# Optimization experiments

Measured on AMD Instinct MI355X. Metric: run time of the kernel, lower is better.

Reference implementation:

```python
import jax, jax.numpy as jnp
import numpy as np

EPS = 1e-8  # torch.cosine_similarity default eps


def setup_inputs() -> dict:
    key = jax.random.key(0)
    k1, k2, k3 = jax.random.split(key, 3)
    B, N, M, C = 8, 2048, 2048, 128
    z = jax.random.randint(k1, (B, N, M), 0, 3, dtype=jnp.int32) - 1  # values in {-1,0,1}
    x1 = jax.random.normal(k2, (B, N, C), dtype=jnp.float32)
    x2 = jax.random.normal(k3, (B, M, C), dtype=jnp.float32)
    s = 10.0
    t = jnp.asarray(s, dtype=jnp.float32)   # nn.Parameter(s)
    b = jnp.asarray(-s, dtype=jnp.float32)  # nn.Parameter(-s)
    return {"z": z, "x1": x1, "x2": x2, "t": t, "b": b}


def reference(z, x1, x2, t, b):
    # cosine similarity as a GEMM instead of broadcast O(B*N*M*C) product:
    # cos = (x1 . x2) / max(||x1|| * ||x2||, eps)  (matches torch.cosine_similarity)
    dots = jnp.einsum('bnc,bmc->bnm', x1, x2)            # [B,N,M]
    n1 = jnp.sqrt(jnp.sum(x1 * x1, axis=-1))             # [B,N]
    n2 = jnp.sqrt(jnp.sum(x2 * x2, axis=-1))             # [B,M]
    denom = jnp.maximum(n1[:, :, None] * n2[:, None, :], EPS)
    cos_sim = dots / denom                               # [B,N,M]

    y = z.astype(jnp.float32) * (t * cos_sim - b)
    mask = z != 0
    nll = -jax.nn.log_sigmoid(y)
    loss = jnp.sum(jnp.where(mask, nll, 0.0)) / jnp.sum(mask).astype(jnp.float32)
    return loss, cos_sim, mask
```

## Files before the change

kernel.cpp:

```cpp
#include <hip/hip_runtime.h>
#include <hip/hip_bf16.h>

#define BATCH 8
#define NDIM  2048
#define MDIM  2048
#define CDIM  128

typedef __attribute__((ext_vector_type(8))) short bf16x8;
typedef __attribute__((ext_vector_type(4))) float f32x4;
typedef __attribute__((ext_vector_type(4), aligned(4))) float f32x4u;

__device__ __forceinline__ float bf2f(unsigned int u16){
    union { unsigned int u; float f; } v; v.u = u16 << 16; return v.f;
}
__device__ __forceinline__ unsigned int f2bf(float f){
    union { float f; unsigned int u; } v; v.f = f;
    unsigned int u = v.u;
    u += 0x7FFFu + ((u >> 16) & 1u);
    return u >> 16;
}

__device__ __forceinline__ void gload_lds16(const void* g, void* l){
    __builtin_amdgcn_global_load_lds(
        (const __attribute__((address_space(1))) void*)g,
        (__attribute__((address_space(3))) void*)l, 16, 0, 0);
}

__global__ void ws_init_kernel(unsigned int* cells){
    cells[threadIdx.x] = 0u;
}

__global__ void finalize_kernel(const float* cells, float* out){
    float s = 0.f;
    int   c = 0;
    #pragma unroll
    for (int i = 0; i < 32; ++i){
        s += cells[i];
        c += ((const int*)cells)[32 + i];
    }
    out[0] = s / (float)c;
}

__global__ __launch_bounds__(256) void prep_kernel(
    const float* __restrict__ x1, const float* __restrict__ x2,
    unsigned short* __restrict__ xb, float* __restrict__ inv)
{
    int gt  = blockIdx.x*256 + threadIdx.x;
    int row = gt >> 4;
    int seg = gt & 15;
    const float* src = (row < 16384) ? (x1 + (size_t)row*128)
                                     : (x2 + (size_t)(row - 16384)*128);
    float4 a = *(const float4*)(src + seg*8);
    float4 b = *(const float4*)(src + seg*8 + 4);
    uint4 pk;
    pk.x = f2bf(a.x) | (f2bf(a.y) << 16);
    pk.y = f2bf(a.z) | (f2bf(a.w) << 16);
    pk.z = f2bf(b.x) | (f2bf(b.y) << 16);
    pk.w = f2bf(b.z) | (f2bf(b.w) << 16);
    ((uint4*)xb)[(size_t)row*16 + seg] = pk;

    float f0 = bf2f(pk.x & 0xffffu), f1 = bf2f(pk.x >> 16);
    float f2 = bf2f(pk.y & 0xffffu), f3 = bf2f(pk.y >> 16);
    float f4 = bf2f(pk.z & 0xffffu), f5 = bf2f(pk.z >> 16);
    float f6 = bf2f(pk.w & 0xffffu), f7 = bf2f(pk.w >> 16);
    float s = f0*f0 + f1*f1 + f2*f2 + f3*f3 + f4*f4 + f5*f5 + f6*f6 + f7*f7;
    s += __shfl_xor(s, 1);
    s += __shfl_xor(s, 2);
    s += __shfl_xor(s, 4);
    s += __shfl_xor(s, 8);
    if (seg == 0) inv[row] = 1.0f / sqrtf(fmaxf(s, 1e-16f));
}

__global__ __launch_bounds__(256, 5) void cossim_bce_fast(
    const int*  __restrict__ zp,
    const unsigned short* __restrict__ xb,
    const float* __restrict__ inv,
    const float* __restrict__ tparm,
    const float* __restrict__ bparm,
    float* __restrict__ out,
    float* __restrict__ cells)
{
    __shared__ __align__(16) unsigned short lB[128*64];

    const int t  = threadIdx.x;
    const int bx = blockIdx.x;
    const int by = blockIdx.y;
    const int bz = blockIdx.z;

    const float tv = *tparm;
    const float bv = *bparm;

    const unsigned short* x1b = xb;
    const unsigned short* x2b = xb + (size_t)16384*128;
    const int x1r0 = bz*NDIM + by*64;
    const int x2r0 = bz*MDIM + bx*128;

    const int lane = t & 63;
    const int w    = t >> 6;
    const int quad = lane >> 4;
    const int l16  = lane & 15;
    const int hi   = lane >> 5;
    const int c4   = lane & 31;

    f32x4 acc[8];
    #pragma unroll
    for (int n = 0; n < 8; ++n)
        acc[n] = (f32x4){0.f, 0.f, 0.f, 0.f};

    const size_t rowBase = (size_t)bz*NDIM*MDIM + (size_t)(by*64 + w*16)*MDIM + (size_t)(bx*128);

    #pragma unroll
    for (int i = 0; i < 4; ++i){
        int chunk = i*256 + t;
        int row = chunk >> 3, pp = chunk & 7;
        int srcpos = pp ^ (row & 7);
        gload_lds16(x2b + ((size_t)(x2r0 + row))*128 + 0*64 + srcpos*8,
                    lB + (size_t)(i*256 + w*64)*8);
    }
    __syncthreads();

    float in1[4], in2[8];
    #pragma unroll
    for (int r = 0; r < 4; ++r) in1[r] = inv[x1r0 + w*16 + quad*4 + r];
    #pragma unroll
    for (int n = 0; n < 8; ++n) in2[n] = inv[16384 + x2r0 + n*16 + l16];

    const unsigned short* aRow = x1b + ((size_t)(x1r0 + w*16 + l16))*128 + quad*8;

    #pragma unroll
    for (int kk = 0; kk < 2; ++kk){
        bf16x8 afr = *(const bf16x8*)(aRow + kk*32);
        const int kc = kk*4 + quad;
        #pragma unroll
        for (int g = 0; g < 2; ++g){
            bf16x8 bfr[4];
            #pragma unroll
            for (int nn = 0; nn < 4; ++nn){
                int brow = (g*4 + nn)*16 + l16;
                bfr[nn] = ((const bf16x8*)lB)[brow*8 + (kc ^ (brow & 7))];
            }
            #pragma unroll
            for (int nn = 0; nn < 4; ++nn)
                acc[g*4+nn] = __builtin_amdgcn_mfma_f32_16x16x32_bf16(
                                afr, bfr[nn], acc[g*4+nn], 0, 0, 0);
        }
    }
    __syncthreads();

    #pragma unroll
    for (int i = 0; i < 4; ++i){
        int chunk = i*256 + t;
        int row = chunk >> 3, pp = chunk & 7;
        int srcpos = pp ^ (row & 7);
        gload_lds16(x2b + ((size_t)(x2r0 + row))*128 + 1*64 + srcpos*8,
                    lB + (size_t)(i*256 + w*64)*8);
    }
    int4 zpre[4];
    #pragma unroll
    for (int i = 0; i < 4; ++i)
        zpre[i] = *(const int4*)(zp + rowBase + (size_t)(i*4 + hi)*MDIM + c4*4);
    __syncthreads();

    #pragma unroll
    for (int kk = 0; kk < 2; ++kk){
        bf16x8 afr = *(const bf16x8*)(aRow + 64 + kk*32);
        const int kc = kk*4 + quad;
        #pragma unroll
        for (int g = 0; g < 2; ++g){
            bf16x8 bfr[4];
            #pragma unroll
            for (int nn = 0; nn < 4; ++nn){
                int brow = (g*4 + nn)*16 + l16;
                bfr[nn] = ((const bf16x8*)lB)[brow*8 + (kc ^ (brow & 7))];
            }
            #pragma unroll
            for (int nn = 0; nn < 4; ++nn)
                acc[g*4+nn] = __builtin_amdgcn_mfma_f32_16x16x32_bf16(
                                afr, bfr[nn], acc[g*4+nn], 0, 0, 0);
        }
    }
    __syncthreads();

    float* scr = (float*)lB + w*1024;
    float* cosOut  = out + 1;
    float* maskOut = out + 1 + (size_t)BATCH*NDIM*MDIM;

    float lnum = 0.f;
    int   lcnt = 0;

    #pragma unroll
    for (int rr = 0; rr < 2; ++rr){
        #pragma unroll
        for (int n = 0; n < 8; ++n){
            #pragma unroll
            for (int j = 0; j < 2; ++j){
                int r  = rr*2 + j;
                int sr = quad*2 + j;
                scr[sr*128 + ((n*16 + l16 + sr*4) & 127)] = acc[n][r] * in1[r] * in2[n];
            }
        }
        #pragma unroll
        for (int i = 0; i < 4; ++i){
            int sr  = i*2 + hi;
            int col = (c4*4 + sr*4) & 127;
            f32x4 cs4 = *(const f32x4*)(scr + sr*128 + col);
            int rowRel = i*4 + rr*2 + hi;
            size_t idx = rowBase + (size_t)rowRel*MDIM + c4*4;

            int4 z4 = zpre[i];
            if (rr == 0)
                zpre[i] = *(const int4*)(zp + idx + (size_t)2*MDIM);

            f32x4 mk;
            float nl = 0.f;
            int   nc = 0;
            #pragma unroll
            for (int j = 0; j < 4; ++j){
                int zv = (&z4.x)[j];
                float cs = cs4[j];
                mk[j] = zv ? 1.0f : 0.0f;
                float y  = (float)zv * (tv*cs - bv);
                float nll = fmaxf(-y, 0.f) + __logf(1.0f + __expf(-fabsf(y)));
                nl += zv ? nll : 0.f;
                nc += zv ? 1 : 0;
            }
            lnum += nl;
            lcnt += nc;
            *(f32x4u*)(cosOut  + idx) = cs4;
            *(f32x4u*)(maskOut + idx) = mk;
        }
    }

    #pragma unroll
    for (int off = 32; off > 0; off >>= 1){
        lnum += __shfl_down(lnum, off);
        lcnt += __shfl_down(lcnt, off);
    }
    __syncthreads();
    float* redf = (float*)lB;
    int*   redi = (int*)lB + 8;
    if (lane == 0){ redf[w] = lnum; redi[w] = lcnt; }
    __syncthreads();
    if (t == 0){
        float s = redf[0] + redf[1] + redf[2] + redf[3];
        int   c = redi[0] + redi[1] + redi[2] + redi[3];
        int cell = (bx + by*16 + bz*512) & 31;
        atomicAdd(cells + cell, s);
        atomicAdd((int*)cells + 32 + cell, c);
    }
}

__global__ __launch_bounds__(256, 5) void cossim_bce_main(
    const int*  __restrict__ zp,
    const float* __restrict__ x1,
    const float* __restrict__ x2,
    const float* __restrict__ tparm,
    const float* __restrict__ bparm,
    float* __restrict__ out,
    float* __restrict__ wsf)
{
    __shared__ __align__(16) unsigned short lds[(64 + 128) * 64];
    __shared__ float nsh[192];
    unsigned short* lA = lds;
    unsigned short* lB = lds + 64*64;

    const int t  = threadIdx.x;
    const int bx = blockIdx.x;
    const int by = blockIdx.y;
    const int bz = blockIdx.z;

    const float tv = *tparm;
    const float bv = *bparm;

    const float* x1base = x1 + ((size_t)(bz*NDIM) + by*64 ) * CDIM;
    const float* x2base = x2 + ((size_t)(bz*MDIM) + bx*128) * CDIM;

    const int lane = t & 63;
    const int w    = t >> 6;
    const int quad = lane >> 4;
    const int l16  = lane & 15;
    const int hi   = lane >> 5;
    const int c4   = lane & 31;

    f32x4 acc[8];
    #pragma unroll
    for (int n = 0; n < 8; ++n)
        acc[n] = (f32x4){0.f, 0.f, 0.f, 0.f};

    float nsum = 0.f;

    #pragma unroll
    for (int ph = 0; ph < 2; ++ph){
        #pragma unroll
        for (int i = 0; i < 6; ++i){
            int chunk = i*256 + t;
            const float* srcb;
            uint4* dst;
            int row, pos;
            if (i < 2){
                row = chunk >> 3; pos = chunk & 7;
                srcb = x1base; dst = (uint4*)lA;
            } else {
                int c2 = chunk - 512;
                row = c2 >> 3; pos = c2 & 7;
                srcb = x2base; dst = (uint4*)lB;
            }
            const float* p = srcb + row*CDIM + ph*64 + pos*8;
            float4 a = *(const float4*)p;
            float4 b = *(const float4*)(p + 4);
            uint4 pk;
            pk.x = f2bf(a.x) | (f2bf(a.y) << 16);
            pk.y = f2bf(a.z) | (f2bf(a.w) << 16);
            pk.z = f2bf(b.x) | (f2bf(b.y) << 16);
            pk.w = f2bf(b.z) | (f2bf(b.w) << 16);
            dst[row*8 + (pos ^ (row & 7))] = pk;
        }
        __syncthreads();

        #pragma unroll
        for (int kk = 0; kk < 2; ++kk){
            const int kc = kk*4 + quad;
            const int arow = w*16 + l16;
            bf16x8 afr = ((const bf16x8*)lA)[arow*8 + (kc ^ (arow & 7))];
            #pragma unroll
            for (int g = 0; g < 2; ++g){
                bf16x8 bfr[4];
                #pragma unroll
                for (int nn = 0; nn < 4; ++nn){
                    int brow = (g*4 + nn)*16 + l16;
                    bfr[nn] = ((const bf16x8*)lB)[brow*8 + (kc ^ (brow & 7))];
                }
                #pragma unroll
                for (int nn = 0; nn < 4; ++nn)
                    acc[g*4+nn] = __builtin_amdgcn_mfma_f32_16x16x32_bf16(
                                    afr, bfr[nn], acc[g*4+nn], 0, 0, 0);
            }
        }

        if (t < 192){
            const uint4* base; int row;
            if (t < 64){ base = (const uint4*)lA; row = t; }
            else       { base = (const uint4*)lB; row = t - 64; }
            #pragma unroll
            for (int c = 0; c < 8; ++c){
                uint4 v = base[row*8 + (c ^ (row & 7))];
                float f0 = bf2f(v.x & 0xffffu), f1 = bf2f(v.x >> 16);
                float f2 = bf2f(v.y & 0xffffu), f3 = bf2f(v.y >> 16);
                float f4 = bf2f(v.z & 0xffffu), f5 = bf2f(v.z >> 16);
                float f6 = bf2f(v.w & 0xffffu), f7 = bf2f(v.w >> 16);
                nsum += f0*f0 + f1*f1 + f2*f2 + f3*f3 + f4*f4 + f5*f5 + f6*f6 + f7*f7;
            }
        }
        __syncthreads();
    }

    if (t < 192) nsh[t] = 1.0f / sqrtf(fmaxf(nsum, 1e-16f));
    __syncthreads();

    float in1[4], in2[8];
    #pragma unroll
    for (int r = 0; r < 4; ++r) in1[r] = nsh[w*16 + quad*4 + r];
    #pragma unroll
    for (int n = 0; n < 8; ++n) in2[n] = nsh[64 + n*16 + l16];

    float* scr = (float*)lds + w*1024;
    float* cosOut  = out + 1;
    float* maskOut = out + 1 + (size_t)BATCH*NDIM*MDIM;
    const size_t rowBase = (size_t)bz*NDIM*MDIM + (size_t)(by*64 + w*16)*MDIM + (size_t)(bx*128);

    float lnum = 0.f;
    int   lcnt = 0;

    int4 zpre[4];
    #pragma unroll
    for (int i = 0; i < 4; ++i)
        zpre[i] = *(const int4*)(zp + rowBase + (size_t)(i*4 + hi)*MDIM + c4*4);

    #pragma unroll
    for (int rr = 0; rr < 2; ++rr){
        #pragma unroll
        for (int n = 0; n < 8; ++n){
            #pragma unroll
            for (int j = 0; j < 2; ++j){
                int r  = rr*2 + j;
                int sr = quad*2 + j;
                scr[sr*128 + ((n*16 + l16 + sr*4) & 127)] = acc[n][r] * in1[r] * in2[n];
            }
        }
        #pragma unroll
        for (int i = 0; i < 4; ++i){
            int sr  = i*2 + hi;
            int col = (c4*4 + sr*4) & 127;
            f32x4 cs4 = *(const f32x4*)(scr + sr*128 + col);
            int rowRel = i*4 + rr*2 + hi;
            size_t idx = rowBase + (size_t)rowRel*MDIM + c4*4;

            int4 z4 = zpre[i];
            if (rr == 0)
                zpre[i] = *(const int4*)(zp + idx + (size_t)2*MDIM);

            f32x4 mk;
            float nl = 0.f;
            int   nc = 0;
            #pragma unroll
            for (int j = 0; j < 4; ++j){
                int zv = (&z4.x)[j];
                float cs = cs4[j];
                mk[j] = zv ? 1.0f : 0.0f;
                float y  = (float)zv * (tv*cs - bv);
                float nll = fmaxf(-y, 0.f) + __logf(1.0f + __expf(-fabsf(y)));
                nl += zv ? nll : 0.f;
                nc += zv ? 1 : 0;
            }
            lnum += nl;
            lcnt += nc;
            *(f32x4u*)(cosOut  + idx) = cs4;
            *(f32x4u*)(maskOut + idx) = mk;
        }
    }

    #pragma unroll
    for (int off = 32; off > 0; off >>= 1){
        lnum += __shfl_down(lnum, off);
        lcnt += __shfl_down(lcnt, off);
    }
    __syncthreads();
    if (lane == 0){ nsh[w] = lnum; ((int*)nsh)[4 + w] = lcnt; }
    __syncthreads();
    if (t == 0){
        float s = nsh[0] + nsh[1] + nsh[2] + nsh[3];
        int   c = ((int*)nsh)[4] + ((int*)nsh)[5] + ((int*)nsh)[6] + ((int*)nsh)[7];
        int cell = (bx + by*16 + bz*512) & 31;
        atomicAdd(wsf + cell, s);
        atomicAdd((int*)wsf + 32 + cell, c);
    }
}

extern "C" void kernel_launch(void* const* d_in, const int* in_sizes, int n_in,
                              void* d_out, int out_size, void* d_ws, size_t ws_size,
                              hipStream_t stream) {
    const int*   zp = (const int*)  d_in[0];
    const float* x1 = (const float*)d_in[1];
    const float* x2 = (const float*)d_in[2];
    const float* tp = (const float*)d_in[3];
    const float* bp = (const float*)d_in[4];
    float* out = (float*)d_out;

    const size_t WS_NEEDED = (size_t)8*1024*1024 + 32768*4 + 256;
    dim3 grid(MDIM/128, NDIM/64, BATCH);

    if (ws_size >= WS_NEEDED){
        unsigned short* xb  = (unsigned short*)d_ws;
        float* inv   = (float*)((char*)d_ws + (size_t)8*1024*1024);
        float* cells = inv + 32768;
        ws_init_kernel<<<1, 64, 0, stream>>>((unsigned int*)cells);
        prep_kernel<<<2048, 256, 0, stream>>>(x1, x2, xb, inv);
        cossim_bce_fast<<<grid, 256, 0, stream>>>(zp, xb, inv, tp, bp, out, cells);
        finalize_kernel<<<1, 1, 0, stream>>>(cells, out);
    } else {
        float* wsf = (float*)d_ws;
        ws_init_kernel<<<1, 64, 0, stream>>>((unsigned int*)d_ws);
        cossim_bce_main<<<grid, 256, 0, stream>>>(zp, x1, x2, tp, bp, out, wsf);
        finalize_kernel<<<1, 1, 0, stream>>>(wsf, out);
    }
}
```

Measured before the change: 123.2 us.

## Load full K tile once, issue z prefetch early, fold ws init into prep

The fast kernel now stages the whole 128x128 bf16 B tile in LDS with one load phase, which removes the second half-K load and one barrier pair. The z tile prefetch is issued before the B loads so its global latency overlaps the GEMM. The inv-norm loads move after the MFMA loop, and the separate workspace-zeroing kernel is merged into the prep kernel, saving one launch. LDS use doubles to 32KB per block, which may lower occupancy below the launch-bounds target. The swizzle only XORs the low 3 bits of a 16-slot row, so bank-conflict behaviour may change.

Result: faster. 118.6 us (-3.8%).

```diff
diff --git a/kernel.cpp b/kernel.cpp
--- a/kernel.cpp
+++ b/kernel.cpp
@@ -26,10 +26,6 @@
         (__attribute__((address_space(3))) void*)l, 16, 0, 0);
 }
 
-__global__ void ws_init_kernel(unsigned int* cells){
-    cells[threadIdx.x] = 0u;
-}
-
 __global__ void finalize_kernel(const float* cells, float* out){
     float s = 0.f;
     int   c = 0;
@@ -43,8 +39,11 @@
 
 __global__ __launch_bounds__(256) void prep_kernel(
     const float* __restrict__ x1, const float* __restrict__ x2,
-    unsigned short* __restrict__ xb, float* __restrict__ inv)
+    unsigned short* __restrict__ xb, float* __restrict__ inv,
+    unsigned int* __restrict__ cells)
 {
+    if (blockIdx.x == 0 && threadIdx.x < 64) cells[threadIdx.x] = 0u;
+
     int gt  = blockIdx.x*256 + threadIdx.x;
     int row = gt >> 4;
     int seg = gt & 15;
@@ -80,7 +79,7 @@
     float* __restrict__ out,
     float* __restrict__ cells)
 {
-    __shared__ __align__(16) unsigned short lB[128*64];
+    __shared__ __align__(16) unsigned short lB[128*128];
 
     const int t  = threadIdx.x;
     const int bx = blockIdx.x;
@@ -109,26 +108,24 @@
 
     const size_t rowBase = (size_t)bz*NDIM*MDIM + (size_t)(by*64 + w*16)*MDIM + (size_t)(bx*128);
 
-    #pragma unroll
-    for (int i = 0; i < 4; ++i){
+    int4 zpre[4];
+    #pragma unroll
+    for (int i = 0; i < 4; ++i)
+        zpre[i] = *(const int4*)(zp + rowBase + (size_t)(i*4 + hi)*MDIM + c4*4);
+
+    #pragma unroll
+    for (int i = 0; i < 8; ++i){
         int chunk = i*256 + t;
-        int row = chunk >> 3, pp = chunk & 7;
+        int row = chunk >> 4, pp = chunk & 15;
         int srcpos = pp ^ (row & 7);
-        gload_lds16(x2b + ((size_t)(x2r0 + row))*128 + 0*64 + srcpos*8,
+        gload_lds16(x2b + ((size_t)(x2r0 + row))*128 + srcpos*8,
                     lB + (size_t)(i*256 + w*64)*8);
     }
     __syncthreads();
 
-    float in1[4], in2[8];
-    #pragma unroll
-    for (int r = 0; r < 4; ++r) in1[r] = inv[x1r0 + w*16 + quad*4 + r];
-    #pragma unroll
-    for (int n = 0; n < 8; ++n) in2[n] = inv[16384 + x2r0 + n*16 + l16];
-
     const unsigned short* aRow = x1b + ((size_t)(x1r0 + w*16 + l16))*128 + quad*8;
-
-    #pragma unroll
-    for (int kk = 0; kk < 2; ++kk){
+    #pragma unroll
+    for (int kk = 0; kk < 4; ++kk){
         bf16x8 afr = *(const bf16x8*)(aRow + kk*32);
         const int kc = kk*4 + quad;
         #pragma unroll
@@ -137,7 +134,7 @@
             #pragma unroll
             for (int nn = 0; nn < 4; ++nn){
                 int brow = (g*4 + nn)*16 + l16;
-                bfr[nn] = ((const bf16x8*)lB)[brow*8 + (kc ^ (brow & 7))];
+                bfr[nn] = ((const bf16x8*)lB)[brow*16 + (kc ^ (brow & 7))];
             }
             #pragma unroll
             for (int nn = 0; nn < 4; ++nn)
@@ -145,40 +142,13 @@
                                 afr, bfr[nn], acc[g*4+nn], 0, 0, 0);
         }
     }
-    __syncthreads();
-
-    #pragma unroll
-    for (int i = 0; i < 4; ++i){
-        int chunk = i*256 + t;
-        int row = chunk >> 3, pp = chunk & 7;
-        int srcpos = pp ^ (row & 7);
-        gload_lds16(x2b + ((size_t)(x2r0 + row))*128 + 1*64 + srcpos*8,
-                    lB + (size_t)(i*256 + w*64)*8);
-    }
-    int4 zpre[4];
-    #pragma unroll
-    for (int i = 0; i < 4; ++i)
-        zpre[i] = *(const int4*)(zp + rowBase + (size_t)(i*4 + hi)*MDIM + c4*4);
-    __syncthreads();
-
-    #pragma unroll
-    for (int kk = 0; kk < 2; ++kk){
-        bf16x8 afr = *(const bf16x8*)(aRow + 64 + kk*32);
-        const int kc = kk*4 + quad;
-        #pragma unroll
-        for (int g = 0; g < 2; ++g){
-            bf16x8 bfr[4];
-            #pragma unroll
-            for (int nn = 0; nn < 4; ++nn){
-                int brow = (g*4 + nn)*16 + l16;
-                bfr[nn] = ((const bf16x8*)lB)[brow*8 + (kc ^ (brow & 7))];
-            }
-            #pragma unroll
-            for (int nn = 0; nn < 4; ++nn)
-                acc[g*4+nn] = __builtin_amdgcn_mfma_f32_16x16x32_bf16(
-                                afr, bfr[nn], acc[g*4+nn], 0, 0, 0);
-        }
-    }
+
+    float in1[4], in2[8];
+    #pragma unroll
+    for (int r = 0; r < 4; ++r) in1[r] = inv[x1r0 + w*16 + quad*4 + r];
+    #pragma unroll
+    for (int n = 0; n < 8; ++n) in2[n] = inv[16384 + x2r0 + n*16 + l16];
+
     __syncthreads();
 
     float* scr = (float*)lB + w*1024;
@@ -248,6 +218,10 @@
         atomicAdd(cells + cell, s);
         atomicAdd((int*)cells + 32 + cell, c);
     }
+}
+
+__global__ void ws_init_kernel(unsigned int* cells){
+    cells[threadIdx.x] = 0u;
 }
 
 __global__ __launch_bounds__(256, 5) void cossim_bce_main(
@@ -453,8 +427,7 @@
         unsigned short* xb  = (unsigned short*)d_ws;
         float* inv   = (float*)((char*)d_ws + (size_t)8*1024*1024);
         float* cells = inv + 32768;
-        ws_init_kernel<<<1, 64, 0, stream>>>((unsigned int*)cells);
-        prep_kernel<<<2048, 256, 0, stream>>>(x1, x2, xb, inv);
+        prep_kernel<<<2048, 256, 0, stream>>>(x1, x2, xb, inv, (unsigned int*)cells);
         cossim_bce_fast<<<grid, 256, 0, stream>>>(zp, xb, inv, tp, bp, out, cells);
         finalize_kernel<<<1, 1, 0, stream>>>(cells, out);
     } else {
```
